# Optimization experiments

Hardware: AMD Instinct MI355X
Metric: run time of the kernel (lower is better)

The kernel has to match this reference:

```python
import jax, jax.numpy as jnp
import numpy as np

B, S, L, D = 64, 512, 6, 512  # batch, seq_len, densely_layer_num, feature dim


def setup_inputs() -> dict:
    key = jax.random.key(0)
    ks = jax.random.split(key, L + 1)
    inp = {f"x{j}": jax.random.normal(ks[j], (B, S, D), dtype=jnp.float32) for j in range(L)}
    # keras initializers.get('normal') -> RandomNormal(stddev=0.05)
    inp["Ws"] = jax.random.normal(ks[L], (S, L, L), dtype=jnp.float32) * 0.05
    return inp


def reference(x0, x1, x2, x3, x4, x5, Ws):
    # Stack densely-connected layer outputs: [B, S, L, D]
    X = jnp.stack([x0, x1, x2, x3, x4, x5], axis=2)
    # Per-position summary over feature dim: [B, S, L]
    s = jnp.sum(X, axis=-1)
    # Per-position (L x L) projection, softmax over layer axis
    logits = jnp.einsum('bsl,slm->bsm', s, Ws)  # [B, S, L]
    a = jax.nn.softmax(logits, axis=-1)
    # Attention-weighted sum over layers: [B, S, D]
    return jnp.einsum('bsl,bsld->bsd', a, X)
```

## Files before the change

kernel.cpp:

```cpp
#include <hip/hip_runtime.h>

constexpr int Bc = 64, Sc = 512, Lc = 6, Dc = 512;

#define KEEP4(v) asm volatile("" : "+v"((v).x), "+v"((v).y), "+v"((v).z), "+v"((v).w))

__global__ __launch_bounds__(256) void densely_att_kernel(
    const float* __restrict__ x0, const float* __restrict__ x1,
    const float* __restrict__ x2, const float* __restrict__ x3,
    const float* __restrict__ x4, const float* __restrict__ x5,
    const float* __restrict__ Ws, float* __restrict__ out)
{
    const int wave = threadIdx.x >> 6;
    const int lane = threadIdx.x & 63;
    const int pair = wave >> 1;
    const int half = wave & 1;

    const long pos = (long)blockIdx.x * 2 + pair;
    const int s_idx = __builtin_amdgcn_readfirstlane((int)(pos % Sc));

    const float* xs[Lc] = {x0, x1, x2, x3, x4, x5};

    const size_t base = (size_t)pos * Dc + (size_t)half * 256 + (size_t)lane * 4;

    float4 v[Lc];
    float ssum[Lc];
    #pragma unroll
    for (int j = 0; j < Lc; ++j) {
        v[j] = *(const float4*)(xs[j] + base);
        KEEP4(v[j]);
        ssum[j] = (v[j].x + v[j].y) + (v[j].z + v[j].w);
    }

    #pragma unroll
    for (int off = 32; off >= 1; off >>= 1) {
        #pragma unroll
        for (int j = 0; j < Lc; ++j)
            ssum[j] += __shfl_xor(ssum[j], off, 64);
    }

    __shared__ float sums[2][2][Lc];
    if (lane == 0) {
        #pragma unroll
        for (int j = 0; j < Lc; ++j) sums[pair][half][j] = ssum[j];
    }
    __syncthreads();
    #pragma unroll
    for (int j = 0; j < Lc; ++j)
        ssum[j] = sums[pair][0][j] + sums[pair][1][j];

    const float* __restrict__ w = Ws + (size_t)s_idx * (Lc * Lc);
    float logits[Lc];
    #pragma unroll
    for (int m = 0; m < Lc; ++m) {
        float acc = 0.f;
        #pragma unroll
        for (int l = 0; l < Lc; ++l)
            acc = fmaf(ssum[l], w[l * Lc + m], acc);
        logits[m] = acc;
    }

    float mx = logits[0];
    #pragma unroll
    for (int m = 1; m < Lc; ++m) mx = fmaxf(mx, logits[m]);
    float a[Lc];
    float denom = 0.f;
    #pragma unroll
    for (int m = 0; m < Lc; ++m) {
        a[m] = __expf(logits[m] - mx);
        denom += a[m];
    }
    const float inv = 1.f / denom;
    #pragma unroll
    for (int m = 0; m < Lc; ++m) a[m] *= inv;

    float4 o = make_float4(0.f, 0.f, 0.f, 0.f);
    #pragma unroll
    for (int j = 0; j < Lc; ++j) {
        o.x = fmaf(a[j], v[j].x, o.x);
        o.y = fmaf(a[j], v[j].y, o.y);
        o.z = fmaf(a[j], v[j].z, o.z);
        o.w = fmaf(a[j], v[j].w, o.w);
    }
    *(float4*)(out + base) = o;
}

extern "C" void kernel_launch(void* const* d_in, const int* in_sizes, int n_in,
                              void* d_out, int out_size, void* d_ws, size_t ws_size,
                              hipStream_t stream) {
    const float* x0 = (const float*)d_in[0];
    const float* x1 = (const float*)d_in[1];
    const float* x2 = (const float*)d_in[2];
    const float* x3 = (const float*)d_in[3];
    const float* x4 = (const float*)d_in[4];
    const float* x5 = (const float*)d_in[5];
    const float* Ws = (const float*)d_in[6];
    float* out = (float*)d_out;

    const int positions = Bc * Sc;
    const int blocks = positions / 2;
    densely_att_kernel<<<blocks, 256, 0, stream>>>(x0, x1, x2, x3, x4, x5, Ws, out);
}
```

Baseline: 349.4 us.

## Map one wave per position, drop LDS sync, use nontemporal stores

Each wave now handles a whole position (all 512 features, as two float4 chunks per lane) instead of two waves splitting it. This removes the shared-memory exchange and the block-wide barrier, and puts twelve vector loads in flight per thread. Output writes become nontemporal stores so they do not pollute the cache. The cost is higher register use per thread and fewer blocks in the grid.

```diff
diff --git a/kernel.cpp b/kernel.cpp
--- a/kernel.cpp
+++ b/kernel.cpp
@@ -2,7 +2,16 @@
 
 constexpr int Bc = 64, Sc = 512, Lc = 6, Dc = 512;
 
-#define KEEP4(v) asm volatile("" : "+v"((v).x), "+v"((v).y), "+v"((v).z), "+v"((v).w))
+typedef float f32x4 __attribute__((ext_vector_type(4)));
+
+#define KEEP12(v)                                                       \
+    asm volatile(""                                                     \
+        : "+v"((v)[0][0]), "+v"((v)[0][1]),                             \
+          "+v"((v)[1][0]), "+v"((v)[1][1]),                             \
+          "+v"((v)[2][0]), "+v"((v)[2][1]),                             \
+          "+v"((v)[3][0]), "+v"((v)[3][1]),                             \
+          "+v"((v)[4][0]), "+v"((v)[4][1]),                             \
+          "+v"((v)[5][0]), "+v"((v)[5][1]))
 
 __global__ __launch_bounds__(256) void densely_att_kernel(
     const float* __restrict__ x0, const float* __restrict__ x1,
@@ -12,23 +21,28 @@
 {
     const int wave = threadIdx.x >> 6;
     const int lane = threadIdx.x & 63;
-    const int pair = wave >> 1;
-    const int half = wave & 1;
 
-    const long pos = (long)blockIdx.x * 2 + pair;
+    const long pos = (long)blockIdx.x * 4 + wave;
     const int s_idx = __builtin_amdgcn_readfirstlane((int)(pos % Sc));
 
     const float* xs[Lc] = {x0, x1, x2, x3, x4, x5};
 
-    const size_t base = (size_t)pos * Dc + (size_t)half * 256 + (size_t)lane * 4;
+    const size_t b0 = (size_t)pos * Dc + (size_t)lane * 4;
+    const size_t b1 = b0 + 256;
 
-    float4 v[Lc];
+    f32x4 v[Lc][2];
+    #pragma unroll
+    for (int j = 0; j < Lc; ++j) {
+        v[j][0] = *(const f32x4*)(xs[j] + b0);
+        v[j][1] = *(const f32x4*)(xs[j] + b1);
+    }
+    KEEP12(v);
+
     float ssum[Lc];
     #pragma unroll
     for (int j = 0; j < Lc; ++j) {
-        v[j] = *(const float4*)(xs[j] + base);
-        KEEP4(v[j]);
-        ssum[j] = (v[j].x + v[j].y) + (v[j].z + v[j].w);
+        f32x4 t = v[j][0] + v[j][1];
+        ssum[j] = (t.x + t.y) + (t.z + t.w);
     }
 
     #pragma unroll
@@ -37,16 +51,6 @@
         for (int j = 0; j < Lc; ++j)
             ssum[j] += __shfl_xor(ssum[j], off, 64);
     }
-
-    __shared__ float sums[2][2][Lc];
-    if (lane == 0) {
-        #pragma unroll
-        for (int j = 0; j < Lc; ++j) sums[pair][half][j] = ssum[j];
-    }
-    __syncthreads();
-    #pragma unroll
-    for (int j = 0; j < Lc; ++j)
-        ssum[j] = sums[pair][0][j] + sums[pair][1][j];
 
     const float* __restrict__ w = Ws + (size_t)s_idx * (Lc * Lc);
     float logits[Lc];
@@ -73,15 +77,15 @@
     #pragma unroll
     for (int m = 0; m < Lc; ++m) a[m] *= inv;
 
-    float4 o = make_float4(0.f, 0.f, 0.f, 0.f);
+    f32x4 o0 = {0.f, 0.f, 0.f, 0.f};
+    f32x4 o1 = {0.f, 0.f, 0.f, 0.f};
     #pragma unroll
     for (int j = 0; j < Lc; ++j) {
-        o.x = fmaf(a[j], v[j].x, o.x);
-        o.y = fmaf(a[j], v[j].y, o.y);
-        o.z = fmaf(a[j], v[j].z, o.z);
-        o.w = fmaf(a[j], v[j].w, o.w);
+        o0 += a[j] * v[j][0];
+        o1 += a[j] * v[j][1];
     }
-    *(float4*)(out + base) = o;
+    __builtin_nontemporal_store(o0, (f32x4*)(out + b0));
+    __builtin_nontemporal_store(o1, (f32x4*)(out + b1));
 }
 
 extern "C" void kernel_launch(void* const* d_in, const int* in_sizes, int n_in,
@@ -97,6 +101,6 @@
     float* out = (float*)d_out;
 
     const int positions = Bc * Sc;
-    const int blocks = positions / 2;
+    const int blocks = positions / 4;
     densely_att_kernel<<<blocks, 256, 0, stream>>>(x0, x1, x2, x3, x4, x5, Ws, out);
 }
```

Measured after the change: 359.8 us. +3.0%, slower.
